# Kernel optimization log

Hardware: AMD Instinct MI355X
Metric: run time of the kernel (lower is better)

The kernel has to match this reference:

```python
import jax, jax.numpy as jnp
import numpy as np

DT = 1.0          # integration timestep (ms)
SIGMA = 0.5       # gauss_std for surrogate (unused in pure fwd spike)
AMPLITUDE = 0.3   # dampening_factor
N = 50000         # neurons
R = 4             # receptor types
D = 5             # max_delay
E = 5000000       # recurrent synapses
B = 4             # batch


def setup_inputs() -> dict:
    key = jax.random.key(0)
    ks = jax.random.split(key, 20)
    f = jnp.float32
    inputs = jax.random.normal(ks[0], (B, N * R), f) * 0.1
    # z_buf holds binary spikes for the last D steps
    z_buf = jax.random.bernoulli(ks[1], 0.05, (B, N * D)).astype(f)
    v = jax.random.uniform(ks[2], (B, N), f, 0.0, 1.0)
    r = jnp.zeros((B, N), f)
    asc_1 = jax.random.normal(ks[3], (B, N), f)
    asc_2 = jax.random.normal(ks[4], (B, N), f)
    psc_rise = jax.random.normal(ks[5], (B, N * R), f) * 0.5
    psc = jax.random.normal(ks[6], (B, N * R), f)
    rec_w = jax.random.normal(ks[7], (E,), f) * 0.01
    rec_rows = jax.random.randint(ks[8], (E,), 0, N * R, jnp.int32)
    rec_cols = jax.random.randint(ks[9], (E,), 0, N * D, jnp.int32)
    syn_decay = jax.random.uniform(ks[10], (N, R), f, 0.5, 0.99)
    psc_initial = jax.random.uniform(ks[11], (N, R), f, 0.1, 1.0)
    t_ref = jax.random.uniform(ks[12], (N,), f, 1.0, 4.0)
    asc_amps = jax.random.normal(ks[13], (N, 2), f)
    k = jax.random.normal(ks[14], (N, 2), f)  # inv-sigmoid space, read via sigmoid
    v_th = jnp.ones((N,), f)
    e_l = jnp.zeros((N,), f)
    v_reset = jnp.zeros((N,), f)
    g = jax.random.uniform(ks[15], (N,), f, 0.1, 1.0)
    decay = jax.random.uniform(ks[16], (N,), f, 0.8, 0.99)
    current_factor = jax.random.uniform(ks[17], (N,), f, 0.1, 1.0)
    voltage_scale = jnp.ones((N,), f) * 20.0
    voltage_offset = jnp.ones((N,), f) * -70.0
    return dict(inputs=inputs, z_buf=z_buf, v=v, r=r, asc_1=asc_1, asc_2=asc_2,
                psc_rise=psc_rise, psc=psc, rec_w=rec_w, rec_rows=rec_rows,
                rec_cols=rec_cols, syn_decay=syn_decay, psc_initial=psc_initial,
                t_ref=t_ref, asc_amps=asc_amps, k=k, v_th=v_th, e_l=e_l,
                v_reset=v_reset, g=g, decay=decay, current_factor=current_factor,
                voltage_scale=voltage_scale, voltage_offset=voltage_offset)


def _step(inputs, z_buf, v, r, asc_1, asc_2, psc_rise, psc,
          rec_w, rec_rows, rec_cols, syn_decay, psc_initial, t_ref,
          asc_amps, k, v_th, e_l, v_reset, g, decay, current_factor,
          voltage_scale, voltage_offset):
    shaped_z_buf = z_buf.reshape(B, D, N)
    prev_z = shaped_z_buf[:, 0]                      # most recent spikes [B,N]
    psc_rise_r = psc_rise.reshape(B, N, R)
    psc_r = psc.reshape(B, N, R)

    # sparse recurrent matmul: W[N*R, N*D] @ z_buf^T -> [N*R, B]
    vals = rec_w[:, None] * z_buf.T[rec_cols]        # [E, B] gather
    i_rec = jax.ops.segment_sum(vals, rec_rows, num_segments=N * R).T  # [B, N*R]

    rec_inputs = (i_rec + inputs).reshape(B, N, R)
    new_psc_rise = syn_decay * psc_rise_r + rec_inputs * psc_initial
    new_psc = psc_r * syn_decay + DT * syn_decay * psc_rise_r

    new_r = jax.nn.relu(r + prev_z * t_ref - DT)

    kk = jax.nn.sigmoid(k)                           # param_k_read()
    new_asc_1 = jnp.exp(-DT * kk[:, 0]) * asc_1 + prev_z * asc_amps[:, 0]
    new_asc_2 = jnp.exp(-DT * kk[:, 1]) * asc_2 + prev_z * asc_amps[:, 1]

    reset_current = prev_z * (v_reset - v_th)
    input_current = psc_r.sum(-1)                    # old psc
    c1 = input_current + asc_1 + asc_2 + g * e_l
    new_v = decay * v + current_factor * c1 + reset_current

    v_sc = (new_v - v_th) / (v_th - e_l)
    new_z = (v_sc > 0.0).astype(v_sc.dtype)          # spike_gauss forward
    new_z = jnp.where(new_r > 0.0, jnp.zeros_like(new_z), new_z)

    new_z_buf = jnp.concatenate([new_z[:, None], shaped_z_buf[:, :-1]], axis=1)
    out_v = new_v * voltage_scale + voltage_offset
    return (new_z, out_v, new_r, new_asc_1, new_asc_2,
            new_psc_rise.reshape(B, N * R), new_psc.reshape(B, N * R),
            new_z_buf.reshape(B, N * D))


def reference(inputs, z_buf, v, r, asc_1, asc_2, psc_rise, psc,
              rec_w, rec_rows, rec_cols, syn_decay, psc_initial, t_ref,
              asc_amps, k, v_th, e_l, v_reset, g, decay, current_factor,
              voltage_scale, voltage_offset):
    outs = _step(inputs, z_buf, v, r, asc_1, asc_2, psc_rise, psc,
                 rec_w, rec_rows, rec_cols, syn_decay, psc_initial, t_ref,
                 asc_amps, k, v_th, e_l, v_reset, g, decay, current_factor,
                 voltage_scale, voltage_offset)
    # pack outputs + new state into one [B, N*(5+2R+D)] array
    return jnp.concatenate(outs, axis=-1)
```

## Files before the change

### kernel.cpp

```cpp
#include <hip/hip_runtime.h>

#define Nn 50000
#define Rr 4
#define Dd 5
#define Ee 5000000
#define Bb 4
#define NRr (Nn * Rr)
#define NDd (Nn * Dd)
#define ZW 7814

struct P {
    const float* inputs; const float* z_buf; const float* v; const float* r;
    const float* asc1; const float* asc2; const float* psc_rise; const float* psc;
    const float* rec_w; const int* rec_rows; const int* rec_cols;
    const float* syn_decay; const float* psc_initial; const float* t_ref;
    const float* asc_amps; const float* k; const float* v_th; const float* e_l;
    const float* v_reset; const float* g; const float* decay;
    const float* current_factor; const float* vscale; const float* voffset;
    float* out; float* i_rec; unsigned char* z_pack; unsigned* zbits;
};

__global__ __launch_bounds__(256) void pack_z_kernel(P p) {
    int i = blockIdx.x * 256 + threadIdx.x;
    if (i < Bb * NRr / 4)
        ((float4*)p.i_rec)[i] = make_float4(0.f, 0.f, 0.f, 0.f);
    unsigned m = 0;
    if (i < NDd) {
#pragma unroll
        for (int b = 0; b < Bb; ++b)
            if (p.z_buf[(size_t)b * NDd + i] != 0.0f) m |= (1u << b);
        p.z_pack[i] = (unsigned char)m;
    }
    unsigned long long bal = __ballot(m != 0);
    if ((i & 63) == 0 && i < NDd) {
        p.zbits[(i >> 5)]     = (unsigned)bal;
        p.zbits[(i >> 5) + 1] = (unsigned)(bal >> 32);
    }
}

__global__ __launch_bounds__(256) void edge_neuron_kernel(P p) {
    __shared__ unsigned zb[ZW];
    for (int t = threadIdx.x; t < ZW; t += 256) zb[t] = p.zbits[t];
    __syncthreads();
    const int tid = blockIdx.x * 256 + threadIdx.x;

    if (tid < Bb * Nn) {
        int b = tid / Nn;
        int n = tid - b * Nn;
        const size_t bn  = (size_t)b * Nn + n;
        const size_t bnr = (size_t)b * NRr + (size_t)n * 4;

        float prev_z = p.z_buf[(size_t)b * NDd + n];
        float4 pr = *(const float4*)(p.psc_rise + bnr);
        float4 pc = *(const float4*)(p.psc + bnr);
        float4 sd = *(const float4*)(p.syn_decay + (size_t)n * 4);

        float4 npc;
        npc.x = pc.x * sd.x + sd.x * pr.x;
        npc.y = pc.y * sd.y + sd.y * pr.y;
        npc.z = pc.z * sd.z + sd.z * pr.z;
        npc.w = pc.w * sd.w + sd.w * pr.w;
        float input_current = pc.x + pc.y + pc.z + pc.w;

        float new_r = fmaxf(p.r[bn] + prev_z * p.t_ref[n] - 1.0f, 0.0f);

        float2 kv = *(const float2*)(p.k + (size_t)n * 2);
        float2 aa = *(const float2*)(p.asc_amps + (size_t)n * 2);
        float kk0 = 1.0f / (1.0f + expf(-kv.x));
        float kk1 = 1.0f / (1.0f + expf(-kv.y));
        float a1 = p.asc1[bn];
        float a2 = p.asc2[bn];
        float na1 = expf(-kk0) * a1 + prev_z * aa.x;
        float na2 = expf(-kk1) * a2 + prev_z * aa.y;

        float vth = p.v_th[n];
        float el  = p.e_l[n];
        float reset_current = prev_z * (p.v_reset[n] - vth);
        float c1 = input_current + a1 + a2 + p.g[n] * el;
        float new_v = p.decay[n] * p.v[bn] + p.current_factor[n] * c1
                      + reset_current;
        float v_sc = (new_v - vth) / (vth - el);
        float new_z = (v_sc > 0.0f) ? 1.0f : 0.0f;
        if (new_r > 0.0f) new_z = 0.0f;
        float out_v = new_v * p.vscale[n] + p.voffset[n];

        float* ob = p.out + (size_t)b * 18 * Nn;
        ob[n]          = new_z;
        ob[Nn + n]     = out_v;
        ob[2 * Nn + n] = new_r;
        ob[3 * Nn + n] = na1;
        ob[4 * Nn + n] = na2;
        *(float4*)(ob + 9 * Nn + (size_t)n * 4) = npc;
        ob[13 * Nn + n] = new_z;
#pragma unroll
        for (int d = 0; d < Dd - 1; ++d)
            ob[14 * Nn + (size_t)d * Nn + n] =
                p.z_buf[(size_t)b * NDd + (size_t)d * Nn + n];
    }

    if (tid < Ee / 4) {
        int4 c = ((const int4*)p.rec_cols)[tid];
        unsigned h0 = (zb[(unsigned)c.x >> 5] >> (c.x & 31)) & 1u;
        unsigned h1 = (zb[(unsigned)c.y >> 5] >> (c.y & 31)) & 1u;
        unsigned h2 = (zb[(unsigned)c.z >> 5] >> (c.z & 31)) & 1u;
        unsigned h3 = (zb[(unsigned)c.w >> 5] >> (c.w & 31)) & 1u;
        if (h0 | h1 | h2 | h3) {
            int4 rw = ((const int4*)p.rec_rows)[tid];
            float4 w = ((const float4*)p.rec_w)[tid];
            float* i_rec = p.i_rec;
            auto do_edge = [&](unsigned hh, int col, int row, float wv) {
                if (hh) {
                    unsigned mm = p.z_pack[col];
                    if (mm & 1u) atomicAdd(&i_rec[0 * NRr + row], wv);
                    if (mm & 2u) atomicAdd(&i_rec[1 * NRr + row], wv);
                    if (mm & 4u) atomicAdd(&i_rec[2 * NRr + row], wv);
                    if (mm & 8u) atomicAdd(&i_rec[3 * NRr + row], wv);
                }
            };
            do_edge(h0, c.x, rw.x, w.x);
            do_edge(h1, c.y, rw.y, w.y);
            do_edge(h2, c.z, rw.z, w.z);
            do_edge(h3, c.w, rw.w, w.w);
        }
    }
}

__global__ __launch_bounds__(256) void psc_rise_kernel(P p) {
    int tid = blockIdx.x * 256 + threadIdx.x;
    if (tid >= Bb * Nn) return;
    int b = tid / Nn;
    int n = tid - b * Nn;
    const size_t bnr = (size_t)b * NRr + (size_t)n * 4;
    float4 ir  = *(const float4*)(p.i_rec + bnr);
    float4 in4 = *(const float4*)(p.inputs + bnr);
    float4 pr  = *(const float4*)(p.psc_rise + bnr);
    float4 sd  = *(const float4*)(p.syn_decay + (size_t)n * 4);
    float4 pi  = *(const float4*)(p.psc_initial + (size_t)n * 4);
    float4 npr;
    npr.x = sd.x * pr.x + (ir.x + in4.x) * pi.x;
    npr.y = sd.y * pr.y + (ir.y + in4.y) * pi.y;
    npr.z = sd.z * pr.z + (ir.z + in4.z) * pi.z;
    npr.w = sd.w * pr.w + (ir.w + in4.w) * pi.w;
    float* ob = p.out + (size_t)b * 18 * Nn;
    *(float4*)(ob + 5 * Nn + (size_t)n * 4) = npr;
}

extern "C" void kernel_launch(void* const* d_in, const int* in_sizes, int n_in,
                              void* d_out, int out_size, void* d_ws, size_t ws_size,
                              hipStream_t stream) {
    P p;
    p.inputs        = (const float*)d_in[0];
    p.z_buf         = (const float*)d_in[1];
    p.v             = (const float*)d_in[2];
    p.r             = (const float*)d_in[3];
    p.asc1          = (const float*)d_in[4];
    p.asc2          = (const float*)d_in[5];
    p.psc_rise      = (const float*)d_in[6];
    p.psc           = (const float*)d_in[7];
    p.rec_w         = (const float*)d_in[8];
    p.rec_rows      = (const int*)d_in[9];
    p.rec_cols      = (const int*)d_in[10];
    p.syn_decay     = (const float*)d_in[11];
    p.psc_initial   = (const float*)d_in[12];
    p.t_ref         = (const float*)d_in[13];
    p.asc_amps      = (const float*)d_in[14];
    p.k             = (const float*)d_in[15];
    p.v_th          = (const float*)d_in[16];
    p.e_l           = (const float*)d_in[17];
    p.v_reset       = (const float*)d_in[18];
    p.g             = (const float*)d_in[19];
    p.decay         = (const float*)d_in[20];
    p.current_factor= (const float*)d_in[21];
    p.vscale        = (const float*)d_in[22];
    p.voffset       = (const float*)d_in[23];
    p.out           = (float*)d_out;
    p.i_rec  = (float*)d_ws;
    p.z_pack = (unsigned char*)d_ws + 3200000;
    p.zbits  = (unsigned*)((char*)d_ws + 3450240);

    pack_z_kernel<<<(NDd + 255) / 256, 256, 0, stream>>>(p);
    edge_neuron_kernel<<<(Ee / 4 + 255) / 256, 256, 0, stream>>>(p);
    psc_rise_kernel<<<(Bb * Nn + 255) / 256, 256, 0, stream>>>(p);
}
```

Measured before the change: 200.3 us.

## Scatter recurrent currents directly into psc_rise output, drop third kernel and bitmask

```diff
diff --git a/kernel.cpp b/kernel.cpp
--- a/kernel.cpp
+++ b/kernel.cpp
@@ -7,7 +7,6 @@
 #define Bb 4
 #define NRr (Nn * Rr)
 #define NDd (Nn * Dd)
-#define ZW 7814
 
 struct P {
     const float* inputs; const float* z_buf; const float* v; const float* r;
@@ -17,31 +16,37 @@
     const float* asc_amps; const float* k; const float* v_th; const float* e_l;
     const float* v_reset; const float* g; const float* decay;
     const float* current_factor; const float* vscale; const float* voffset;
-    float* out; float* i_rec; unsigned char* z_pack; unsigned* zbits;
+    float* out; unsigned char* z_pack;
 };
 
-__global__ __launch_bounds__(256) void pack_z_kernel(P p) {
+__global__ __launch_bounds__(256) void pack_base_kernel(P p) {
     int i = blockIdx.x * 256 + threadIdx.x;
-    if (i < Bb * NRr / 4)
-        ((float4*)p.i_rec)[i] = make_float4(0.f, 0.f, 0.f, 0.f);
-    unsigned m = 0;
     if (i < NDd) {
+        unsigned m = 0;
 #pragma unroll
         for (int b = 0; b < Bb; ++b)
             if (p.z_buf[(size_t)b * NDd + i] != 0.0f) m |= (1u << b);
         p.z_pack[i] = (unsigned char)m;
     }
-    unsigned long long bal = __ballot(m != 0);
-    if ((i & 63) == 0 && i < NDd) {
-        p.zbits[(i >> 5)]     = (unsigned)bal;
-        p.zbits[(i >> 5) + 1] = (unsigned)(bal >> 32);
+    if (i < Bb * Nn) {
+        int b = i / Nn;
+        int n = i - b * Nn;
+        const size_t bnr = (size_t)b * NRr + (size_t)n * 4;
+        float4 pr  = *(const float4*)(p.psc_rise + bnr);
+        float4 in4 = *(const float4*)(p.inputs + bnr);
+        float4 sd  = *(const float4*)(p.syn_decay + (size_t)n * 4);
+        float4 pi  = *(const float4*)(p.psc_initial + (size_t)n * 4);
+        float4 base;
+        base.x = sd.x * pr.x + in4.x * pi.x;
+        base.y = sd.y * pr.y + in4.y * pi.y;
+        base.z = sd.z * pr.z + in4.z * pi.z;
+        base.w = sd.w * pr.w + in4.w * pi.w;
+        float* ob = p.out + (size_t)b * 18 * Nn;
+        *(float4*)(ob + 5 * Nn + (size_t)n * 4) = base;
     }
 }
 
 __global__ __launch_bounds__(256) void edge_neuron_kernel(P p) {
-    __shared__ unsigned zb[ZW];
-    for (int t = threadIdx.x; t < ZW; t += 256) zb[t] = p.zbits[t];
-    __syncthreads();
     const int tid = blockIdx.x * 256 + threadIdx.x;
 
     if (tid < Bb * Nn) {
@@ -100,49 +105,30 @@
 
     if (tid < Ee / 4) {
         int4 c = ((const int4*)p.rec_cols)[tid];
-        unsigned h0 = (zb[(unsigned)c.x >> 5] >> (c.x & 31)) & 1u;
-        unsigned h1 = (zb[(unsigned)c.y >> 5] >> (c.y & 31)) & 1u;
-        unsigned h2 = (zb[(unsigned)c.z >> 5] >> (c.z & 31)) & 1u;
-        unsigned h3 = (zb[(unsigned)c.w >> 5] >> (c.w & 31)) & 1u;
-        if (h0 | h1 | h2 | h3) {
+        unsigned m0 = p.z_pack[c.x];
+        unsigned m1 = p.z_pack[c.y];
+        unsigned m2 = p.z_pack[c.z];
+        unsigned m3 = p.z_pack[c.w];
+        if (m0 | m1 | m2 | m3) {
             int4 rw = ((const int4*)p.rec_rows)[tid];
             float4 w = ((const float4*)p.rec_w)[tid];
-            float* i_rec = p.i_rec;
-            auto do_edge = [&](unsigned hh, int col, int row, float wv) {
-                if (hh) {
-                    unsigned mm = p.z_pack[col];
-                    if (mm & 1u) atomicAdd(&i_rec[0 * NRr + row], wv);
-                    if (mm & 2u) atomicAdd(&i_rec[1 * NRr + row], wv);
-                    if (mm & 4u) atomicAdd(&i_rec[2 * NRr + row], wv);
-                    if (mm & 8u) atomicAdd(&i_rec[3 * NRr + row], wv);
+            float* out5 = p.out + 5 * Nn;
+            auto do_edge = [&](unsigned mm, int row, float wv) {
+                if (mm) {
+                    float s = wv * p.psc_initial[row];
+                    float* o = out5 + row;
+                    if (mm & 1u) atomicAdd(o, s);
+                    if (mm & 2u) atomicAdd(o + 18 * Nn, s);
+                    if (mm & 4u) atomicAdd(o + 36 * Nn, s);
+                    if (mm & 8u) atomicAdd(o + 54 * Nn, s);
                 }
             };
-            do_edge(h0, c.x, rw.x, w.x);
-            do_edge(h1, c.y, rw.y, w.y);
-            do_edge(h2, c.z, rw.z, w.z);
-            do_edge(h3, c.w, rw.w, w.w);
+            do_edge(m0, rw.x, w.x);
+            do_edge(m1, rw.y, w.y);
+            do_edge(m2, rw.z, w.z);
+            do_edge(m3, rw.w, w.w);
         }
     }
-}
-
-__global__ __launch_bounds__(256) void psc_rise_kernel(P p) {
-    int tid = blockIdx.x * 256 + threadIdx.x;
-    if (tid >= Bb * Nn) return;
-    int b = tid / Nn;
-    int n = tid - b * Nn;
-    const size_t bnr = (size_t)b * NRr + (size_t)n * 4;
-    float4 ir  = *(const float4*)(p.i_rec + bnr);
-    float4 in4 = *(const float4*)(p.inputs + bnr);
-    float4 pr  = *(const float4*)(p.psc_rise + bnr);
-    float4 sd  = *(const float4*)(p.syn_decay + (size_t)n * 4);
-    float4 pi  = *(const float4*)(p.psc_initial + (size_t)n * 4);
-    float4 npr;
-    npr.x = sd.x * pr.x + (ir.x + in4.x) * pi.x;
-    npr.y = sd.y * pr.y + (ir.y + in4.y) * pi.y;
-    npr.z = sd.z * pr.z + (ir.z + in4.z) * pi.z;
-    npr.w = sd.w * pr.w + (ir.w + in4.w) * pi.w;
-    float* ob = p.out + (size_t)b * 18 * Nn;
-    *(float4*)(ob + 5 * Nn + (size_t)n * 4) = npr;
 }
 
 extern "C" void kernel_launch(void* const* d_in, const int* in_sizes, int n_in,
@@ -174,11 +160,8 @@
     p.vscale        = (const float*)d_in[22];
     p.voffset       = (const float*)d_in[23];
     p.out           = (float*)d_out;
-    p.i_rec  = (float*)d_ws;
-    p.z_pack = (unsigned char*)d_ws + 3200000;
-    p.zbits  = (unsigned*)((char*)d_ws + 3450240);
+    p.z_pack = (unsigned char*)d_ws;
 
-    pack_z_kernel<<<(NDd + 255) / 256, 256, 0, stream>>>(p);
+    pack_base_kernel<<<(NDd + 255) / 256, 256, 0, stream>>>(p);
     edge_neuron_kernel<<<(Ee / 4 + 255) / 256, 256, 0, stream>>>(p);
-    psc_rise_kernel<<<(Bb * Nn + 255) / 256, 256, 0, stream>>>(p);
 }
```

After: 209.2 us. 1.04x slower.
